# Performance work log

Hardware: AMD Instinct MI355X
Metric: run time of the kernel (lower is better)

## Reference

```python
import jax, jax.numpy as jnp
import numpy as np

L = 16384      # sequence length
D_IN = 512     # d_input
D_H = 1024     # d_hidden
D_OUT = 512    # d_output
R_MIN = 0.0
R_MAX = 0.99
MAX_PHASE = np.pi


def setup_inputs() -> dict:
    key = jax.random.key(0)
    k_nu, k_th, k_x, k_bre, k_bim, k_cre, k_cim, k_d = jax.random.split(key, 8)
    # nu_init with parametrization='exp'
    u_nu = jax.random.uniform(k_nu, (D_H,), dtype=jnp.float32)
    nu = jnp.sqrt(u_nu * (R_MAX ** 2 - R_MIN ** 2) + R_MIN ** 2)
    u_theta = jax.random.uniform(k_th, (D_H,), dtype=jnp.float32, minval=-MAX_PHASE, maxval=MAX_PHASE)
    theta = jnp.mod(u_theta, 2 * jnp.pi)
    lamb = jnp.stack([jnp.log(-jnp.log(nu)), jnp.log(theta)], axis=0)  # [2, D_H]
    # gamma_init with parametrization='exp': nu = exp(-exp(lamb[0]))
    nu_eff = jnp.exp(-jnp.exp(lamb[0]))
    gamma = jnp.log(jnp.sqrt(1.0 - jnp.abs(nu_eff) ** 2))  # [D_H]
    # matrix_init: normal / sqrt(shape[0])
    B_re = jax.random.normal(k_bre, (D_H, D_IN), dtype=jnp.float32) / jnp.sqrt(D_H)
    B_im = jax.random.normal(k_bim, (D_H, D_IN), dtype=jnp.float32) / jnp.sqrt(D_H)
    C_re = jax.random.normal(k_cre, (D_OUT, D_H), dtype=jnp.float32) / jnp.sqrt(D_OUT)
    C_im = jax.random.normal(k_cim, (D_OUT, D_H), dtype=jnp.float32) / jnp.sqrt(D_OUT)
    D = jax.random.normal(k_d, (D_OUT, D_IN), dtype=jnp.float32) / jnp.sqrt(D_OUT)
    inputs = jax.random.normal(k_x, (L, D_IN), dtype=jnp.float32)
    return {"inputs": inputs, "lamb": lamb, "gamma": gamma,
            "B_re": B_re, "B_im": B_im, "C_re": C_re, "C_im": C_im, "D": D}


def _binary_operator_diag(q_i, q_j):
    A_i, b_i = q_i
    A_j, b_j = q_j
    return (A_j * A_i, A_j * b_i + b_j)


def reference(inputs, lamb, gamma, B_re, B_im, C_re, C_im, D):
    # parametrization='exp': lambda = exp(-exp(nu_log) + i*exp(theta_log))
    diag_lambda = jnp.exp(-jnp.exp(lamb[0]) + 1j * jnp.exp(lamb[1]))  # [D_H] complex64
    # which_gamma='learned', exp param: scale rows of B by exp(gamma)
    B_norm = jnp.exp(gamma)[:, None] * (B_re + 1j * B_im)             # [D_H, D_IN]
    # Bu_t = B_norm @ x_t for all t, as one GEMM: [L, D_H] complex
    Bu = inputs.astype(B_norm.dtype) @ B_norm.T
    Lambda_elements = jnp.broadcast_to(diag_lambda[None, :], Bu.shape)
    # diagonal linear recurrence h_t = lambda*h_{t-1} + Bu_t via parallel scan
    _, h = jax.lax.associative_scan(_binary_operator_diag, (Lambda_elements, Bu))
    C = C_re + 1j * C_im
    # y_t = Re[C h_t] + D x_t
    outputs = jnp.real(h @ C.T) + inputs @ D.T  # [L, D_OUT]
    return outputs
```

## Files before the change

kernel.cpp:

```cpp
#include <hip/hip_runtime.h>

__device__ __forceinline__ unsigned short f2b(float f) {
    unsigned int u = __builtin_bit_cast(unsigned int, f);
    unsigned int r = (u + 0x7FFFu + ((u >> 16) & 1u)) >> 16;
    return (unsigned short)r;
}
__device__ __forceinline__ float b2f(unsigned short s) {
    unsigned int u = ((unsigned int)s) << 16;
    return __builtin_bit_cast(float, u);
}

typedef __attribute__((ext_vector_type(8))) short short8;
typedef __attribute__((ext_vector_type(4))) float float4v;

#define GLD16(g, l) __builtin_amdgcn_global_load_lds(                          \
    (const __attribute__((address_space(1))) unsigned int*)(g),                \
    (__attribute__((address_space(3))) unsigned int*)(l), 16, 0, 0)

#define WAIT_VM12() __builtin_amdgcn_s_waitcnt(0x0F7C)
#define WAIT_VM0()  __builtin_amdgcn_s_waitcnt(0x0F70)

#define SEQLEN 16384
#define NCHUNK 512
#define TCHUNK 32
#define LDH 2560

__global__ void prep_all(const float* __restrict__ x,
                         const float* __restrict__ B_re, const float* __restrict__ B_im,
                         const float* __restrict__ gamma,
                         const float* __restrict__ C_re, const float* __restrict__ C_im,
                         const float* __restrict__ Dm,
                         unsigned short* __restrict__ Hcat,
                         unsigned short* __restrict__ Bcat,
                         unsigned short* __restrict__ CW) {
    int b = blockIdx.x;
    if (b < 8192) {
        int id = b * 256 + threadIdx.x;
        int t = id >> 7;
        int k4 = (id & 127) << 2;
        float4 v = *(const float4*)(x + (long)t * 512 + k4);
        ushort4 o;
        o.x = f2b(v.x); o.y = f2b(v.y); o.z = f2b(v.z); o.w = f2b(v.w);
        *(ushort4*)(Hcat + (long)t * LDH + 2048 + k4) = o;
    } else if (b < 9216) {
        int id = (b - 8192) * 256 + threadIdx.x;
        int n = id >> 7;
        int k4 = (id & 127) << 2;
        const float* src = (n < 1024) ? (B_re + (long)n * 512) : (B_im + (long)(n - 1024) * 512);
        float g = expf(gamma[n & 1023]);
        float4 v = *(const float4*)(src + k4);
        ushort4 o;
        o.x = f2b(v.x * g); o.y = f2b(v.y * g); o.z = f2b(v.z * g); o.w = f2b(v.w * g);
        *(ushort4*)(Bcat + (long)n * 512 + k4) = o;
    } else {
        int id = (b - 9216) * 256 + threadIdx.x;
        int o = id / 640;
        int j4 = (id - o * 640) << 2;
        float4 v; float sgn = 1.0f;
        if (j4 < 1024) {
            v = *(const float4*)(C_re + (long)o * 1024 + j4);
        } else if (j4 < 2048) {
            v = *(const float4*)(C_im + (long)o * 1024 + (j4 - 1024));
            sgn = -1.0f;
        } else {
            v = *(const float4*)(Dm + (long)o * 512 + (j4 - 2048));
        }
        ushort4 w;
        w.x = f2b(v.x * sgn); w.y = f2b(v.y * sgn); w.z = f2b(v.z * sgn); w.w = f2b(v.w * sgn);
        *(ushort4*)(CW + (long)o * 2560 + j4) = w;
    }
}

template <bool OUT_BF16>
__launch_bounds__(64)
__global__ void gemm_w64(const unsigned short* __restrict__ A, int lda,
                         const unsigned short* __restrict__ B, int ldb,
                         void* __restrict__ Cout, int ldc, int Ktot,
                         int nbx_shift) {
    __shared__ unsigned short sm[3][6144] __attribute__((aligned(16)));
    const int lane = threadIdx.x;

    const int bid = blockIdx.x;
    const int xcd = bid & 7;
    const int g = bid >> 3;
    const int bx = g & ((1 << nbx_shift) - 1);
    const int by = xcd * 32 + (g >> nbx_shift);
    const long m0 = (long)by * 64;
    const long n0 = (long)bx * 128;

    const unsigned short* Ag = A + (m0 + (lane >> 2)) * lda + (lane & 3) * 8;
    const unsigned short* Bg = B + (n0 + (lane >> 2)) * ldb + (lane & 3) * 8;

    const int fr = lane & 15;
    const int fk = (lane >> 4) * 8;

    float4v acc[4][8] = {};
    short8 faE[4], fbE[8], faO[4], fbO[8];

    unsigned short* p0 = sm[0];
    unsigned short* p1 = sm[1];
    unsigned short* p2 = sm[2];

    auto stage = [&](unsigned short* buf, int k0) {
#pragma unroll
        for (int i = 0; i < 4; i++)
            GLD16(Ag + (long)i * 16 * lda + k0, buf + i * 512);
#pragma unroll
        for (int j = 0; j < 8; j++)
            GLD16(Bg + (long)j * 16 * ldb + k0, buf + 2048 + j * 512);
    };
    auto loadfrags = [&](const unsigned short* buf, short8* fa, short8* fb) {
#pragma unroll
        for (int i = 0; i < 4; i++)
            fa[i] = *(const short8*)(buf + (i * 16 + fr) * 32 + fk);
#pragma unroll
        for (int j = 0; j < 8; j++)
            fb[j] = *(const short8*)(buf + 2048 + (j * 16 + fr) * 32 + fk);
    };
    auto domfma = [&](const short8* fa, const short8* fb) {
#pragma unroll
        for (int mi = 0; mi < 4; mi++)
#pragma unroll
            for (int ni = 0; ni < 8; ni++)
                acc[mi][ni] = __builtin_amdgcn_mfma_f32_16x16x32_bf16(fa[mi], fb[ni], acc[mi][ni], 0, 0, 0);
    };

    const int nk = Ktot >> 5;

    stage(p0, 0);
    stage(p1, 32);
    WAIT_VM12();
    loadfrags(p0, faE, fbE);

    int k0 = 0;
    for (int i = 0; i < nk - 2; i += 2) {
        stage(p2, k0 + 64);
        WAIT_VM12();
        loadfrags(p1, faO, fbO);
        domfma(faE, fbE);
        { unsigned short* t = p0; p0 = p1; p1 = p2; p2 = t; }
        k0 += 32;
        stage(p2, k0 + 64);
        WAIT_VM12();
        loadfrags(p1, faE, fbE);
        domfma(faO, fbO);
        { unsigned short* t = p0; p0 = p1; p1 = p2; p2 = t; }
        k0 += 32;
    }
    WAIT_VM0();
    loadfrags(p1, faO, fbO);
    domfma(faE, fbE);
    domfma(faO, fbO);

    const int er = (lane >> 4) * 4;
    const int ec = lane & 15;
#pragma unroll
    for (int mi = 0; mi < 4; mi++) {
#pragma unroll
        for (int r = 0; r < 4; r++) {
            long grow = m0 + mi * 16 + er + r;
#pragma unroll
            for (int ni = 0; ni < 8; ni++) {
                long gcol = n0 + ni * 16 + ec;
                float v = acc[mi][ni][r];
                if (OUT_BF16)
                    ((unsigned short*)Cout)[grow * ldc + gcol] = f2b(v);
                else
                    ((float*)Cout)[grow * ldc + gcol] = v;
            }
        }
    }
}

__global__ void scan_ends(const unsigned short* __restrict__ Hcat,
                          const float* __restrict__ lamb,
                          float* __restrict__ E) {
    const int chunk = blockIdx.x;
    const int ch = threadIdx.x << 2;
    float lre[4], lim[4];
#pragma unroll
    for (int i = 0; i < 4; i++) {
        float nu = expf(-expf(lamb[ch + i]));
        float th = expf(lamb[1024 + ch + i]);
        lre[i] = nu * cosf(th);
        lim[i] = nu * sinf(th);
    }
    float hr[4] = {0, 0, 0, 0}, hi[4] = {0, 0, 0, 0};
    const unsigned short* base = Hcat + (long)chunk * TCHUNK * LDH + ch;
#pragma unroll 4
    for (int t = 0; t < TCHUNK; t++) {
        ushort4 br = *(const ushort4*)(base + (long)t * LDH);
        ushort4 bi = *(const ushort4*)(base + (long)t * LDH + 1024);
        float brf[4] = {b2f(br.x), b2f(br.y), b2f(br.z), b2f(br.w)};
        float bif[4] = {b2f(bi.x), b2f(bi.y), b2f(bi.z), b2f(bi.w)};
#pragma unroll
        for (int i = 0; i < 4; i++) {
            float nr = fmaf(lre[i], hr[i], fmaf(-lim[i], hi[i], brf[i]));
            float ni = fmaf(lre[i], hi[i], fmaf(lim[i], hr[i], bif[i]));
            hr[i] = nr; hi[i] = ni;
        }
    }
    float* Ec = E + (long)chunk * 2048 + ch;
#pragma unroll
    for (int i = 0; i < 4; i++) {
        Ec[i] = hr[i];
        Ec[1024 + i] = hi[i];
    }
}

__global__ void carry(const float* __restrict__ lamb, const float* __restrict__ E,
                      float* __restrict__ Kc) {
    const int ch = blockIdx.x * 256 + threadIdx.x;
    double nu = exp(-exp((double)lamb[ch]));
    double th = exp((double)lamb[1024 + ch]);
    double lr = nu * cos(th), li = nu * sin(th);
#pragma unroll
    for (int i = 0; i < 5; i++) {
        double rr = lr * lr - li * li;
        double ii = 2.0 * lr * li;
        lr = rr; li = ii;
    }
    float tre = (float)lr, tim = (float)li;
    float hr = 0.0f, hi = 0.0f;
#pragma unroll 8
    for (int c = 0; c < NCHUNK; c++) {
        Kc[(long)c * 2048 + ch] = hr;
        Kc[(long)c * 2048 + 1024 + ch] = hi;
        float er = E[(long)c * 2048 + ch];
        float ei = E[(long)c * 2048 + 1024 + ch];
        float nr = fmaf(tre, hr, fmaf(-tim, hi, er));
        float ni = fmaf(tre, hi, fmaf(tim, hr, ei));
        hr = nr; hi = ni;
    }
}

__global__ void scan_apply(unsigned short* __restrict__ Hcat,
                           const float* __restrict__ lamb,
                           const float* __restrict__ Kc) {
    const int chunk = blockIdx.x;
    const int ch = threadIdx.x << 2;
    float lre[4], lim[4];
#pragma unroll
    for (int i = 0; i < 4; i++) {
        float nu = expf(-expf(lamb[ch + i]));
        float th = expf(lamb[1024 + ch + i]);
        lre[i] = nu * cosf(th);
        lim[i] = nu * sinf(th);
    }
    float hr[4], hi[4];
#pragma unroll
    for (int i = 0; i < 4; i++) {
        hr[i] = Kc[(long)chunk * 2048 + ch + i];
        hi[i] = Kc[(long)chunk * 2048 + 1024 + ch + i];
    }
    unsigned short* base = Hcat + (long)chunk * TCHUNK * LDH + ch;
#pragma unroll 4
    for (int t = 0; t < TCHUNK; t++) {
        ushort4 br = *(const ushort4*)(base + (long)t * LDH);
        ushort4 bi = *(const ushort4*)(base + (long)t * LDH + 1024);
        float brf[4] = {b2f(br.x), b2f(br.y), b2f(br.z), b2f(br.w)};
        float bif[4] = {b2f(bi.x), b2f(bi.y), b2f(bi.z), b2f(bi.w)};
#pragma unroll
        for (int i = 0; i < 4; i++) {
            float nr = fmaf(lre[i], hr[i], fmaf(-lim[i], hi[i], brf[i]));
            float ni = fmaf(lre[i], hi[i], fmaf(lim[i], hr[i], bif[i]));
            hr[i] = nr; hi[i] = ni;
        }
        ushort4 orv, oiv;
        orv.x = f2b(hr[0]); orv.y = f2b(hr[1]); orv.z = f2b(hr[2]); orv.w = f2b(hr[3]);
        oiv.x = f2b(hi[0]); oiv.y = f2b(hi[1]); oiv.z = f2b(hi[2]); oiv.w = f2b(hi[3]);
        *(ushort4*)(base + (long)t * LDH) = orv;
        *(ushort4*)(base + (long)t * LDH + 1024) = oiv;
    }
}

extern "C" void kernel_launch(void* const* d_in, const int* in_sizes, int n_in,
                              void* d_out, int out_size, void* d_ws, size_t ws_size,
                              hipStream_t stream) {
    const float* x     = (const float*)d_in[0];
    const float* lamb  = (const float*)d_in[1];
    const float* gamma = (const float*)d_in[2];
    const float* B_re  = (const float*)d_in[3];
    const float* B_im  = (const float*)d_in[4];
    const float* C_re  = (const float*)d_in[5];
    const float* C_im  = (const float*)d_in[6];
    const float* Dm    = (const float*)d_in[7];

    char* ws = (char*)d_ws;
    unsigned short* Hcat = (unsigned short*)ws;
    float* E  = (float*)(ws + 83886080);
    float* Kc = E + (long)NCHUNK * 2048;
    unsigned short* Bcat = (unsigned short*)((char*)Kc + 4194304);
    unsigned short* CW   = Bcat + (long)2048 * 512;

    prep_all<<<10496, 256, 0, stream>>>(x, B_re, B_im, gamma, C_re, C_im, Dm, Hcat, Bcat, CW);
    gemm_w64<true><<<4096, 64, 0, stream>>>(Hcat + 2048, LDH, Bcat, 512, Hcat, LDH, 512,
                                            4);
    scan_ends<<<NCHUNK, 256, 0, stream>>>(Hcat, lamb, E);
    carry<<<4, 256, 0, stream>>>(lamb, E, Kc);
    scan_apply<<<NCHUNK, 256, 0, stream>>>(Hcat, lamb, Kc);
    gemm_w64<false><<<1024, 64, 0, stream>>>(Hcat, LDH, CW, 2560, (float*)d_out, 512, 2560,
                                             2);
}
```

Measured before the change: 286.8 us.

## Replace single-wave 64x128 GEMM with 4-wave 128x128 block-tiled GEMM

Swaps the one-wavefront GEMM kernel, which used a triple-buffered 64x128 tile and manual waitcnt pipelining, for a 256-thread block computing a 128x128 tile. Four waves share double-buffered LDS tiles and synchronise with __syncthreads, and each wave owns a 64x64 subtile. The goal is more operand reuse per LDS load and higher occupancy through launch bounds. In exchange it adds block-wide barriers every K step and relies on the compiler to insert the vmcnt waits, so load/compute overlap may get worse.

```diff
diff --git a/kernel.cpp b/kernel.cpp
--- a/kernel.cpp
+++ b/kernel.cpp
@@ -16,9 +16,6 @@
 #define GLD16(g, l) __builtin_amdgcn_global_load_lds(                          \
     (const __attribute__((address_space(1))) unsigned int*)(g),                \
     (__attribute__((address_space(3))) unsigned int*)(l), 16, 0, 0)
-
-#define WAIT_VM12() __builtin_amdgcn_s_waitcnt(0x0F7C)
-#define WAIT_VM0()  __builtin_amdgcn_s_waitcnt(0x0F70)
 
 #define SEQLEN 16384
 #define NCHUNK 512
@@ -72,85 +69,67 @@
 }
 
 template <bool OUT_BF16>
-__launch_bounds__(64)
-__global__ void gemm_w64(const unsigned short* __restrict__ A, int lda,
-                         const unsigned short* __restrict__ B, int ldb,
-                         void* __restrict__ Cout, int ldc, int Ktot,
-                         int nbx_shift) {
-    __shared__ unsigned short sm[3][6144] __attribute__((aligned(16)));
-    const int lane = threadIdx.x;
+__launch_bounds__(256, 3)
+__global__ void gemm_t128(const unsigned short* __restrict__ A, int lda,
+                          const unsigned short* __restrict__ B, int ldb,
+                          void* __restrict__ Cout, int ldc, int Ktot,
+                          int nbx_shift) {
+    __shared__ unsigned short sm[2][8192] __attribute__((aligned(16)));
+    const int lane = threadIdx.x & 63;
+    const int wid = threadIdx.x >> 6;
 
     const int bid = blockIdx.x;
     const int xcd = bid & 7;
     const int g = bid >> 3;
     const int bx = g & ((1 << nbx_shift) - 1);
-    const int by = xcd * 32 + (g >> nbx_shift);
-    const long m0 = (long)by * 64;
+    const int by = xcd * (gridDim.x >> (3 + nbx_shift)) + (g >> nbx_shift);
+    const long m0 = (long)by * 128;
     const long n0 = (long)bx * 128;
 
-    const unsigned short* Ag = A + (m0 + (lane >> 2)) * lda + (lane & 3) * 8;
-    const unsigned short* Bg = B + (n0 + (lane >> 2)) * ldb + (lane & 3) * 8;
+    const int srow = lane >> 2;
+    const int scol = (lane & 3) * 8;
+    const unsigned short* Ag = A + (m0 + wid * 32 + srow) * (long)lda + scol;
+    const unsigned short* Bg = B + (n0 + wid * 32 + srow) * (long)ldb + scol;
 
     const int fr = lane & 15;
     const int fk = (lane >> 4) * 8;
-
-    float4v acc[4][8] = {};
-    short8 faE[4], fbE[8], faO[4], fbO[8];
-
-    unsigned short* p0 = sm[0];
-    unsigned short* p1 = sm[1];
-    unsigned short* p2 = sm[2];
+    const int wr = (wid >> 1) * 64;
+    const int wc = (wid & 1) * 64;
+
+    float4v acc[4][4] = {};
+    short8 fa[4], fb[4];
 
     auto stage = [&](unsigned short* buf, int k0) {
+        GLD16(Ag + k0, buf + wid * 1024);
+        GLD16(Ag + (long)16 * lda + k0, buf + wid * 1024 + 512);
+        GLD16(Bg + k0, buf + 4096 + wid * 1024);
+        GLD16(Bg + (long)16 * ldb + k0, buf + 4096 + wid * 1024 + 512);
+    };
+    auto loadfrags = [&](const unsigned short* buf) {
 #pragma unroll
         for (int i = 0; i < 4; i++)
-            GLD16(Ag + (long)i * 16 * lda + k0, buf + i * 512);
-#pragma unroll
-        for (int j = 0; j < 8; j++)
-            GLD16(Bg + (long)j * 16 * ldb + k0, buf + 2048 + j * 512);
+            fa[i] = *(const short8*)(buf + (wr + i * 16 + fr) * 32 + fk);
+#pragma unroll
+        for (int j = 0; j < 4; j++)
+            fb[j] = *(const short8*)(buf + 4096 + (wc + j * 16 + fr) * 32 + fk);
     };
-    auto loadfrags = [&](const unsigned short* buf, short8* fa, short8* fb) {
-#pragma unroll
-        for (int i = 0; i < 4; i++)
-            fa[i] = *(const short8*)(buf + (i * 16 + fr) * 32 + fk);
-#pragma unroll
-        for (int j = 0; j < 8; j++)
-            fb[j] = *(const short8*)(buf + 2048 + (j * 16 + fr) * 32 + fk);
-    };
-    auto domfma = [&](const short8* fa, const short8* fb) {
+
+    const int nk = Ktot >> 5;
+    unsigned short* pc = sm[0];
+    unsigned short* pn = sm[1];
+    stage(pc, 0);
+#pragma unroll 2
+    for (int t = 0; t < nk; ++t) {
+        __syncthreads();
+        if (t + 1 < nk) stage(pn, (t + 1) * 32);
+        loadfrags(pc);
 #pragma unroll
         for (int mi = 0; mi < 4; mi++)
 #pragma unroll
-            for (int ni = 0; ni < 8; ni++)
+            for (int ni = 0; ni < 4; ni++)
                 acc[mi][ni] = __builtin_amdgcn_mfma_f32_16x16x32_bf16(fa[mi], fb[ni], acc[mi][ni], 0, 0, 0);
-    };
-
-    const int nk = Ktot >> 5;
-
-    stage(p0, 0);
-    stage(p1, 32);
-    WAIT_VM12();
-    loadfrags(p0, faE, fbE);
-
-    int k0 = 0;
-    for (int i = 0; i < nk - 2; i += 2) {
-        stage(p2, k0 + 64);
-        WAIT_VM12();
-        loadfrags(p1, faO, fbO);
-        domfma(faE, fbE);
-        { unsigned short* t = p0; p0 = p1; p1 = p2; p2 = t; }
-        k0 += 32;
-        stage(p2, k0 + 64);
-        WAIT_VM12();
-        loadfrags(p1, faE, fbE);
-        domfma(faO, fbO);
-        { unsigned short* t = p0; p0 = p1; p1 = p2; p2 = t; }
-        k0 += 32;
-    }
-    WAIT_VM0();
-    loadfrags(p1, faO, fbO);
-    domfma(faE, fbE);
-    domfma(faO, fbO);
+        unsigned short* t2 = pc; pc = pn; pn = t2;
+    }
 
     const int er = (lane >> 4) * 4;
     const int ec = lane & 15;
@@ -158,10 +137,10 @@
     for (int mi = 0; mi < 4; mi++) {
 #pragma unroll
         for (int r = 0; r < 4; r++) {
-            long grow = m0 + mi * 16 + er + r;
-#pragma unroll
-            for (int ni = 0; ni < 8; ni++) {
-                long gcol = n0 + ni * 16 + ec;
+            long grow = m0 + wr + mi * 16 + er + r;
+#pragma unroll
+            for (int ni = 0; ni < 4; ni++) {
+                long gcol = n0 + wc + ni * 16 + ec;
                 float v = acc[mi][ni][r];
                 if (OUT_BF16)
                     ((unsigned short*)Cout)[grow * ldc + gcol] = f2b(v);
@@ -294,11 +273,11 @@
     unsigned short* CW   = Bcat + (long)2048 * 512;
 
     prep_all<<<10496, 256, 0, stream>>>(x, B_re, B_im, gamma, C_re, C_im, Dm, Hcat, Bcat, CW);
-    gemm_w64<true><<<4096, 64, 0, stream>>>(Hcat + 2048, LDH, Bcat, 512, Hcat, LDH, 512,
-                                            4);
+    gemm_t128<true><<<2048, 256, 0, stream>>>(Hcat + 2048, LDH, Bcat, 512, Hcat, LDH, 512,
+                                              4);
     scan_ends<<<NCHUNK, 256, 0, stream>>>(Hcat, lamb, E);
     carry<<<4, 256, 0, stream>>>(lamb, E, Kc);
     scan_apply<<<NCHUNK, 256, 0, stream>>>(Hcat, lamb, Kc);
-    gemm_w64<false><<<1024, 64, 0, stream>>>(Hcat, LDH, CW, 2560, (float*)d_out, 512, 2560,
-                                             2);
-}
+    gemm_t128<false><<<512, 256, 0, stream>>>(Hcat, LDH, CW, 2560, (float*)d_out, 512, 2560,
+                                              2);
+}
```

Result: faster. 271.7 us (-5.2%).
